# Optimization experiments

Hardware: AMD Instinct MI355X
Metric: run time of the kernel (lower is better)

## Reference

```python
import jax, jax.numpy as jnp
import numpy as np

B, N, K, NUM_CLASSES = 8, 4096, 16, 40
M = B * N


def _safe_norm(v):
    s = jnp.sum(v * v, axis=-1)
    return jnp.where(s > 0, jnp.sqrt(jnp.where(s > 0, s, 1.0)), 0.0)


def _angle(v1, v2):
    cn = _safe_norm(jnp.cross(v1, v2))
    d = jnp.sum(v1 * v2, axis=-1)
    ok = (cn > 0) | (d != 0)
    return jnp.where(ok, jnp.arctan2(cn, jnp.where(ok, d, 1.0)), 0.0)


def _ppf(pos_i, pos_j, n_i, n_j):
    # PyG point_pair_features: pseudo = pos_j - pos_i (j = source, i = target)
    pseudo = pos_j - pos_i
    return jnp.stack([_safe_norm(pseudo), _angle(n_i, pseudo),
                      _angle(n_j, pseudo), _angle(n_i, n_j)], axis=-1)


def _knn_edges(pos):
    # knn_graph(k=K, loop=False), per-graph; returns (src, dst) with self-loops
    # appended (PPFConv add_self_loops=True default).
    p = pos.reshape(B, N, 3)
    sq = jnp.sum(p * p, axis=-1)                                   # [B,N]
    d2 = sq[:, :, None] + sq[:, None, :] - 2.0 * jnp.einsum('bnd,bmd->bnm', p, p)
    d2 = jnp.where(jnp.eye(N, dtype=bool)[None], jnp.inf, d2)      # no loops
    _, nbr = jax.lax.top_k(-d2, K)                                  # [B,N,K]
    offs = (jnp.arange(B) * N)[:, None, None]
    src = (nbr + offs).reshape(-1)                                  # neighbors j
    dst = jnp.repeat(jnp.arange(M), K)                              # targets i
    loops = jnp.arange(M)
    return jnp.concatenate([src, loops]), jnp.concatenate([dst, loops])


def _mlp(e, w1, b1, w2, b2):
    return jax.nn.relu(e @ w1 + b1) @ w2 + b2


def setup_inputs() -> dict:
    key = jax.random.key(0)
    ks = jax.random.split(key, 12)
    pos = jax.random.normal(ks[0], (M, 3), jnp.float32)
    nrm = jax.random.normal(ks[1], (M, 3), jnp.float32)
    nrm = nrm / jnp.linalg.norm(nrm, axis=-1, keepdims=True)
    batch = jnp.repeat(jnp.arange(B, dtype=jnp.int32), N)
    s = 0.1
    return {
        'pos': pos, 'normal': nrm, 'batch': batch,
        'w1a': jax.random.normal(ks[2], (4, 32)) * s,  'b1a': jnp.zeros(32),
        'w1b': jax.random.normal(ks[3], (32, 32)) * s, 'b1b': jnp.zeros(32),
        'w2a': jax.random.normal(ks[4], (36, 32)) * s, 'b2a': jnp.zeros(32),
        'w2b': jax.random.normal(ks[5], (32, 32)) * s, 'b2b': jnp.zeros(32),
        'wc':  jax.random.normal(ks[6], (32, NUM_CLASSES)) * s,
        'bc':  jnp.zeros(NUM_CLASSES),
    }


def reference(pos, normal, batch, w1a, b1a, w1b, b1b, w2a, b2a, w2b, b2b, wc, bc):
    src, dst = _knn_edges(pos)
    feats = _ppf(pos[dst], pos[src], normal[dst], normal[src])      # [E,4]
    # conv1: x=None -> message = mlp1(ppf), scatter-max per target node
    msg1 = _mlp(feats, w1a, b1a, w1b, b1b)
    x = jax.nn.relu(jax.ops.segment_max(msg1, dst, num_segments=M))  # [M,32]
    # conv2: message = mlp2([x_j, ppf])
    msg2 = _mlp(jnp.concatenate([x[src], feats], axis=-1), w2a, b2a, w2b, b2b)
    x = jax.nn.relu(jax.ops.segment_max(msg2, dst, num_segments=M))
    # global_max_pool over each graph (uniform batch: reshape)
    g = x.reshape(B, N, 32).max(axis=1)                              # [B,32]
    return g @ wc + bc                                               # [B,40]
```

## Files before the change

### kernel.cpp

```cpp
#include <hip/hip_runtime.h>
#include <hip/hip_bf16.h>
#include <math.h>

#define NB 8
#define NN 4096
#define KK 16
#define MM (NB*NN)
#define CH 32
#define SLOTS 17
#define NCLS 40
#define BIG 3.0e38f
#define CAP 96
#define NBLK2 (MM/8)
#define HROW 36

#define OW1A 0
#define OB1A 128
#define OW1B 160
#define OB1B 1184
#define OW2A 1216
#define OB2A 2368
#define OW2B 2400
#define OB2B 3424
#define OWC  3456
#define OBC  4736
#define NWTS 4776

typedef short short8 __attribute__((ext_vector_type(8)));
typedef float f32x4  __attribute__((ext_vector_type(4)));

__device__ float4 g_pos4[MM];
__device__ float4 g_nrm4[MM];
__device__ int    g_nbr[MM*KK];
__device__ float  g_u[MM*CH];
__device__ float  g_bmax[NBLK2*CH];
__device__ float  g_wts[NWTS];
__device__ __align__(16) unsigned short g_wfrag1[2][2][64][8];
__device__ __align__(16) unsigned short g_wfrag2[2][2][64][8];
__device__ int    g_isf32;

__device__ __forceinline__ float bf(const __hip_bfloat16 x) { return __bfloat162float(x); }

__device__ __forceinline__ float ldf(const void* p, int i, bool f32) {
  return f32 ? ((const float*)p)[i] : bf(((const __hip_bfloat16*)p)[i]);
}

__device__ __forceinline__ float angf(float ax, float ay, float az,
                                      float bx, float by, float bz) {
  float cx = ay*bz - az*by;
  float cy = az*bx - ax*bz;
  float cz = ax*by - ay*bx;
  float s  = cx*cx + cy*cy + cz*cz;
  float cn = s > 0.f ? sqrtf(s) : 0.f;
  float d  = ax*bx + ay*by + az*bz;
  return (cn > 0.f || d != 0.f) ? atan2f(cn, d) : 0.f;
}

__device__ __forceinline__ void ppf4(const float4 pi, const float4 ni,
                                     const float4 pj, const float4 nj, float* f) {
  float px = pj.x - pi.x, py = pj.y - pi.y, pz = pj.z - pi.z;
  float s = px*px + py*py + pz*pz;
  f[0] = s > 0.f ? sqrtf(s) : 0.f;
  f[1] = angf(ni.x, ni.y, ni.z, px, py, pz);
  f[2] = angf(nj.x, nj.y, nj.z, px, py, pz);
  f[3] = angf(ni.x, ni.y, ni.z, nj.x, nj.y, nj.z);
}

__device__ __forceinline__ unsigned int fkey(float f) {
  unsigned int u = __float_as_uint(f);
  return (u & 0x80000000u) ? ~u : (u | 0x80000000u);
}
__device__ __forceinline__ float funkey(unsigned int k) {
  unsigned int u = (k & 0x80000000u) ? (k ^ 0x80000000u) : ~k;
  return __uint_as_float(u);
}

__device__ __forceinline__ void bsplit(float v, unsigned short* hi, unsigned short* lo) {
  __hip_bfloat16 h = __float2bfloat16(v);
  float hf = __bfloat162float(h);
  __hip_bfloat16 l = __float2bfloat16(v - hf);
  *hi = *reinterpret_cast<unsigned short*>(&h);
  *lo = *reinterpret_cast<unsigned short*>(&l);
}

__device__ __forceinline__ void afrag(const float* row, short8* ah, short8* al) {
  float4 a = *(const float4*)row;
  float4 b = *(const float4*)(row + 4);
  unsigned short h, l;
  #pragma unroll
  for (int j = 0; j < 4; ++j) {
    bsplit((&a.x)[j], &h, &l); (*ah)[j]   = (short)h; (*al)[j]   = (short)l;
    bsplit((&b.x)[j], &h, &l); (*ah)[j+4] = (short)h; (*al)[j+4] = (short)l;
  }
}

__global__ __launch_bounds__(256) void wprep_kernel(
    const void* nrm, const void* w1a, const void* b1a, const void* w1b,
    const void* b1b, const void* w2a, const void* b2a, const void* w2b,
    const void* b2b, const void* wc, const void* bc) {
  __shared__ int sflag;
  const int tid = threadIdx.x;
  if (tid < 64) {
    const float* nf = (const float*)nrm;
    const __hip_bfloat16* nh = (const __hip_bfloat16*)nrm;
    float x = nf[3*tid], y = nf[3*tid+1], z = nf[3*tid+2];
    float ss = x*x + y*y + z*z;
    bool okf = (ss > 0.98f && ss < 1.02f);
    float a = bf(nh[3*tid]), b2 = bf(nh[3*tid+1]), c2 = bf(nh[3*tid+2]);
    float sb = a*a + b2*b2 + c2*c2;
    bool okb = (sb > 0.95f && sb < 1.05f);
    unsigned long long mf = __ballot(okf), mb = __ballot(okb);
    if (tid == 0) {
      sflag = (__popcll(mf) >= __popcll(mb)) ? 1 : 0;
      g_isf32 = sflag;
    }
  }
  __syncthreads();
  const bool f32 = sflag != 0;
  for (int i = tid; i < 128;  i += 256) g_wts[OW1A + i] = ldf(w1a, i, f32);
  for (int i = tid; i < 32;   i += 256) g_wts[OB1A + i] = ldf(b1a, i, f32);
  for (int i = tid; i < 1024; i += 256) g_wts[OW1B + i] = ldf(w1b, i, f32);
  for (int i = tid; i < 32;   i += 256) g_wts[OB1B + i] = ldf(b1b, i, f32);
  for (int i = tid; i < 1152; i += 256) g_wts[OW2A + i] = ldf(w2a, i, f32);
  for (int i = tid; i < 32;   i += 256) g_wts[OB2A + i] = ldf(b2a, i, f32);
  for (int i = tid; i < 1024; i += 256) g_wts[OW2B + i] = ldf(w2b, i, f32);
  for (int i = tid; i < 32;   i += 256) g_wts[OB2B + i] = ldf(b2b, i, f32);
  for (int i = tid; i < 1280; i += 256) g_wts[OWC  + i] = ldf(wc,  i, f32);
  for (int i = tid; i < 40;   i += 256) g_wts[OBC  + i] = ldf(bc,  i, f32);
  for (int i = tid; i < 4096; i += 256) {
    int which = i >> 11;
    int r = i & 2047;
    int t  = r >> 10;  r &= 1023;
    int hl = r >> 9;   r &= 511;
    int ln = r >> 3;
    int j  = r & 7;
    int k = (ln >> 4)*8 + j;
    int c = t*16 + (ln & 15);
    float wv = ldf(which ? w2b : w1b, k*CH + c, f32);
    unsigned short hi, lo;
    bsplit(wv, &hi, &lo);
    unsigned short v = hl ? lo : hi;
    if (which) g_wfrag2[t][hl][ln][j] = v;
    else       g_wfrag1[t][hl][ln][j] = v;
  }
}

__global__ __launch_bounds__(256) void prep_kernel(const void* __restrict__ pos,
                                                   const void* __restrict__ nrm) {
  const bool f32 = g_isf32 != 0;
  int i = blockIdx.x*256 + threadIdx.x;
  float x = ldf(pos, 3*i, f32), y = ldf(pos, 3*i+1, f32), z = ldf(pos, 3*i+2, f32);
  float sq = x*x + y*y + z*z;
  g_pos4[i] = make_float4(x, y, z, sq);
  float a = ldf(nrm, 3*i, f32), b = ldf(nrm, 3*i+1, f32), c = ldf(nrm, 3*i+2, f32);
  g_nrm4[i] = make_float4(a, b, c, 0.f);
}

__global__ __launch_bounds__(512) void knn_kernel() {
  __shared__ float sx[NN], sy[NN], sz[NN];
  __shared__ unsigned short ilst[64][CAP];
  __shared__ double dlst[8][CAP];
  __shared__ int    cnt[64];
  const int tid  = threadIdx.x;
  const int w    = tid >> 6, lane = tid & 63;
  const int blk  = blockIdx.x;
  const int b    = blk >> 6;
  const int qbw  = ((blk & 63) << 6) | (w << 3);
  const float4* bp = g_pos4 + b*NN;

  #pragma unroll
  for (int k = 0; k < 8; ++k) {
    int idx = k*512 + tid;
    float4 o = bp[idx];
    sx[idx] = o.x; sy[idx] = o.y; sz[idx] = o.z;
  }
  __syncthreads();

  float q2x[8], q2y[8], q2z[8];
  #pragma unroll
  for (int qq = 0; qq < 8; ++qq) {
    int qi = qbw + qq;
    q2x[qq] = -2.f*sx[qi]; q2y[qq] = -2.f*sy[qi]; q2z[qq] = -2.f*sz[qi];
  }

  float mn[8];
  #pragma unroll
  for (int qq = 0; qq < 8; ++qq) mn[qq] = BIG;
  #pragma unroll 4
  for (int it = 0; it < 64; ++it) {
    int idx = it*64 + lane;
    float ox = sx[idx], oy = sy[idx], oz = sz[idx];
    float ow = __builtin_fmaf(oz, oz, __builtin_fmaf(oy, oy, ox*ox));
    #pragma unroll
    for (int qq = 0; qq < 8; ++qq) {
      float d = __builtin_fmaf(q2x[qq], ox,
                __builtin_fmaf(q2y[qq], oy,
                __builtin_fmaf(q2z[qq], oz, ow)));
      mn[qq] = fminf(mn[qq], d);
    }
  }

  unsigned int key[8], lo[8], hi[8];
  #pragma unroll
  for (int qq = 0; qq < 8; ++qq) { key[qq] = fkey(mn[qq]); lo[qq] = 0u; hi[qq] = 0xFFFFFFFFu; }
  #pragma unroll 1
  for (int s = 0; s < 32; ++s) {
    #pragma unroll
    for (int qq = 0; qq < 8; ++qq) {
      unsigned int mid = lo[qq] + ((hi[qq] - lo[qq]) >> 1);
      int c = (int)__popcll(__ballot(key[qq] <= mid));
      if (c >= 17) hi[qq] = mid; else lo[qq] = mid + 1;
    }
  }
  float Tf[8];
  #pragma unroll
  for (int qq = 0; qq < 8; ++qq) {
    float T = funkey(hi[qq]);
    Tf[qq] = T + 4e-5f + 1e-5f*fabsf(T);
  }

  if (lane < 8) cnt[(w<<3) | lane] = 0;

  #pragma unroll 4
  for (int it = 0; it < 64; ++it) {
    int idx = it*64 + lane;
    float ox = sx[idx], oy = sy[idx], oz = sz[idx];
    float ow = __builtin_fmaf(oz, oz, __builtin_fmaf(oy, oy, ox*ox));
    #pragma unroll
    for (int qq = 0; qq < 8; ++qq) {
      float d = __builtin_fmaf(q2x[qq], ox,
                __builtin_fmaf(q2y[qq], oy,
                __builtin_fmaf(q2z[qq], oz, ow)));
      if (d <= Tf[qq] && idx != qbw + qq) {
        int p = atomicAdd(&cnt[(w<<3)|qq], 1);
        if (p < CAP) ilst[(w<<3)|qq][p] = (unsigned short)idx;
      }
    }
  }

  #pragma unroll 1
  for (int qq = 0; qq < 8; ++qq) {
    const int qi = qbw + qq;
    const int m = min(cnt[(w<<3)|qq], CAP);
    const double mx = (double)sx[qi], my_ = (double)sy[qi], mz = (double)sz[qi];
    const double sqme = (mx*mx + my_*my_) + mz*mz;
    for (int e = lane; e < m; e += 64) {
      int ci = ilst[(w<<3)|qq][e];
      double ox = (double)sx[ci], oy = (double)sy[ci], oz = (double)sz[ci];
      double sqo = (ox*ox + oy*oy) + oz*oz;
      double dt  = (mx*ox + my_*oy) + mz*oz;
      dlst[w][e] = (sqme + sqo) - 2.0*dt;
    }
    for (int e = lane; e < m; e += 64) {
      double myd = dlst[w][e];
      int myi = ilst[(w<<3)|qq][e];
      int rank = 0;
      for (int o = 0; o < m; ++o) {
        double od = dlst[w][o];
        int oi = ilst[(w<<3)|qq][o];
        rank += (od < myd) || (od == myd && oi < myi);
      }
      if (rank < KK) g_nbr[(b*NN + qi)*KK + rank] = b*NN + myi;
    }
  }
}

__global__ __launch_bounds__(256) void conv1_kernel() {
  __shared__ __align__(16) float fe[136][4];
  __shared__ __align__(16) float h1s[152*HROW];
  __shared__ __align__(16) float wsaT[32*HROW];
  __shared__ float xs[8][CH];
  const int tid = threadIdx.x;
  const int c = tid & 31;
  const int lane = tid & 63, wv = tid >> 6;
  const int quad = lane >> 4, l15 = lane & 15;
  const int node0 = blockIdx.x << 3;
  float w1a_c[4];
  #pragma unroll
  for (int f = 0; f < 4; ++f) w1a_c[f] = g_wts[OW1A + f*CH + c];
  const float b1a_c = g_wts[OB1A + c];
  short8 bH0 = *(const short8*)&g_wfrag1[0][0][lane][0];
  short8 bL0 = *(const short8*)&g_wfrag1[0][1][lane][0];
  short8 bH1 = *(const short8*)&g_wfrag1[1][0][lane][0];
  short8 bL1 = *(const short8*)&g_wfrag1[1][1][lane][0];
  const float bias0 = g_wts[OB1B + l15];
  const float bias1 = g_wts[OB1B + 16 + l15];

  for (int i = tid; i < 1024; i += 256) {
    int k = i >> 5, cc = i & 31;
    wsaT[cc*HROW + k] = g_wts[OW2A + i];
  }
  if (tid < 136) {
    int ns = tid / 17, slot = tid - ns*17;
    int i = node0 + ns;
    int j = (slot < KK) ? g_nbr[i*KK + slot] : i;
    ppf4(g_pos4[i], g_nrm4[i], g_pos4[j], g_nrm4[j], fe[tid]);
  }
  __syncthreads();
  #pragma unroll
  for (int it = 0; it < 17; ++it) {
    int idx = it*256 + tid;
    int e = idx >> 5;
    float4 f4 = *(const float4*)fe[e];
    float h = b1a_c + f4.x*w1a_c[0] + f4.y*w1a_c[1] + f4.z*w1a_c[2] + f4.w*w1a_c[3];
    h1s[e*HROW + c] = fmaxf(h, 0.f);
  }
  __syncthreads();
  #pragma unroll
  for (int ni = 0; ni < 2; ++ni) {
    const int n8 = wv*2 + ni;
    const int rbase = n8*17;
    short8 ah0, al0, ah1, al1;
    afrag(&h1s[(rbase      + l15)*HROW + quad*8], &ah0, &al0);
    afrag(&h1s[(rbase + 16 + l15)*HROW + quad*8], &ah1, &al1);
    f32x4 a00 = {0.f,0.f,0.f,0.f}, a01 = a00, a10 = a00, a11 = a00;
    a00 = __builtin_amdgcn_mfma_f32_16x16x32_bf16(ah0, bH0, a00, 0, 0, 0);
    a00 = __builtin_amdgcn_mfma_f32_16x16x32_bf16(ah0, bL0, a00, 0, 0, 0);
    a00 = __builtin_amdgcn_mfma_f32_16x16x32_bf16(al0, bH0, a00, 0, 0, 0);
    a01 = __builtin_amdgcn_mfma_f32_16x16x32_bf16(ah0, bH1, a01, 0, 0, 0);
    a01 = __builtin_amdgcn_mfma_f32_16x16x32_bf16(ah0, bL1, a01, 0, 0, 0);
    a01 = __builtin_amdgcn_mfma_f32_16x16x32_bf16(al0, bH1, a01, 0, 0, 0);
    a10 = __builtin_amdgcn_mfma_f32_16x16x32_bf16(ah1, bH0, a10, 0, 0, 0);
    a10 = __builtin_amdgcn_mfma_f32_16x16x32_bf16(ah1, bL0, a10, 0, 0, 0);
    a10 = __builtin_amdgcn_mfma_f32_16x16x32_bf16(al1, bH0, a10, 0, 0, 0);
    a11 = __builtin_amdgcn_mfma_f32_16x16x32_bf16(ah1, bH1, a11, 0, 0, 0);
    a11 = __builtin_amdgcn_mfma_f32_16x16x32_bf16(ah1, bL1, a11, 0, 0, 0);
    a11 = __builtin_amdgcn_mfma_f32_16x16x32_bf16(al1, bH1, a11, 0, 0, 0);
    float m0 = fmaxf(fmaxf(a00[0], a00[1]), fmaxf(a00[2], a00[3]));
    float m1 = fmaxf(fmaxf(a01[0], a01[1]), fmaxf(a01[2], a01[3]));
    if (quad == 0) { m0 = fmaxf(m0, a10[0]); m1 = fmaxf(m1, a11[0]); }
    m0 = fmaxf(m0, __shfl_xor(m0, 16)); m0 = fmaxf(m0, __shfl_xor(m0, 32));
    m1 = fmaxf(m1, __shfl_xor(m1, 16)); m1 = fmaxf(m1, __shfl_xor(m1, 32));
    if (quad == 0) {
      xs[n8][l15]      = fmaxf(m0 + bias0, 0.f);
      xs[n8][16 + l15] = fmaxf(m1 + bias1, 0.f);
    }
  }
  __syncthreads();
  const int ns = tid >> 5;
  float uu = 0.f;
  #pragma unroll
  for (int k4 = 0; k4 < 8; ++k4) {
    float4 x4 = *(const float4*)&xs[ns][4*k4];
    float4 w4 = *(const float4*)&wsaT[c*HROW + 4*k4];
    uu += x4.x*w4.x + x4.y*w4.y + x4.z*w4.z + x4.w*w4.w;
  }
  g_u[(node0 + ns)*CH + c] = uu;
}

__global__ __launch_bounds__(256) void conv2_kernel() {
  __shared__ __align__(16) float fe[136][4];
  __shared__ int jn[136];
  __shared__ __align__(16) float h1s[152*HROW];
  __shared__ float xs[8][CH];
  const int tid = threadIdx.x;
  const int c = tid & 31;
  const int lane = tid & 63, wv = tid >> 6;
  const int quad = lane >> 4, l15 = lane & 15;
  const int node0 = blockIdx.x << 3;
  float w2aL_c[4];
  #pragma unroll
  for (int f = 0; f < 4; ++f) w2aL_c[f] = g_wts[OW2A + (CH + f)*CH + c];
  const float b2a_c = g_wts[OB2A + c];
  short8 bH0 = *(const short8*)&g_wfrag2[0][0][lane][0];
  short8 bL0 = *(const short8*)&g_wfrag2[0][1][lane][0];
  short8 bH1 = *(const short8*)&g_wfrag2[1][0][lane][0];
  short8 bL1 = *(const short8*)&g_wfrag2[1][1][lane][0];
  const float bias0 = g_wts[OB2B + l15];
  const float bias1 = g_wts[OB2B + 16 + l15];

  if (tid < 136) {
    int ns = tid / 17, slot = tid - ns*17;
    int i = node0 + ns;
    int j = (slot < KK) ? g_nbr[i*KK + slot] : i;
    jn[tid] = j;
    ppf4(g_pos4[i], g_nrm4[i], g_pos4[j], g_nrm4[j], fe[tid]);
  }
  __syncthreads();
  #pragma unroll
  for (int it = 0; it < 17; ++it) {
    int idx = it*256 + tid;
    int e = idx >> 5;
    float4 f4 = *(const float4*)fe[e];
    float uv = g_u[jn[e]*CH + c];
    float h = b2a_c + uv + f4.x*w2aL_c[0] + f4.y*w2aL_c[1] + f4.z*w2aL_c[2] + f4.w*w2aL_c[3];
    h1s[e*HROW + c] = fmaxf(h, 0.f);
  }
  __syncthreads();
  #pragma unroll
  for (int ni = 0; ni < 2; ++ni) {
    const int n8 = wv*2 + ni;
    const int rbase = n8*17;
    short8 ah0, al0, ah1, al1;
    afrag(&h1s[(rbase      + l15)*HROW + quad*8], &ah0, &al0);
    afrag(&h1s[(rbase + 16 + l15)*HROW + quad*8], &ah1, &al1);
    f32x4 a00 = {0.f,0.f,0.f,0.f}, a01 = a00, a10 = a00, a11 = a00;
    a00 = __builtin_amdgcn_mfma_f32_16x16x32_bf16(ah0, bH0, a00, 0, 0, 0);
    a00 = __builtin_amdgcn_mfma_f32_16x16x32_bf16(ah0, bL0, a00, 0, 0, 0);
    a00 = __builtin_amdgcn_mfma_f32_16x16x32_bf16(al0, bH0, a00, 0, 0, 0);
    a01 = __builtin_amdgcn_mfma_f32_16x16x32_bf16(ah0, bH1, a01, 0, 0, 0);
    a01 = __builtin_amdgcn_mfma_f32_16x16x32_bf16(ah0, bL1, a01, 0, 0, 0);
    a01 = __builtin_amdgcn_mfma_f32_16x16x32_bf16(al0, bH1, a01, 0, 0, 0);
    a10 = __builtin_amdgcn_mfma_f32_16x16x32_bf16(ah1, bH0, a10, 0, 0, 0);
    a10 = __builtin_amdgcn_mfma_f32_16x16x32_bf16(ah1, bL0, a10, 0, 0, 0);
    a10 = __builtin_amdgcn_mfma_f32_16x16x32_bf16(al1, bH0, a10, 0, 0, 0);
    a11 = __builtin_amdgcn_mfma_f32_16x16x32_bf16(ah1, bH1, a11, 0, 0, 0);
    a11 = __builtin_amdgcn_mfma_f32_16x16x32_bf16(ah1, bL1, a11, 0, 0, 0);
    a11 = __builtin_amdgcn_mfma_f32_16x16x32_bf16(al1, bH1, a11, 0, 0, 0);
    float m0 = fmaxf(fmaxf(a00[0], a00[1]), fmaxf(a00[2], a00[3]));
    float m1 = fmaxf(fmaxf(a01[0], a01[1]), fmaxf(a01[2], a01[3]));
    if (quad == 0) { m0 = fmaxf(m0, a10[0]); m1 = fmaxf(m1, a11[0]); }
    m0 = fmaxf(m0, __shfl_xor(m0, 16)); m0 = fmaxf(m0, __shfl_xor(m0, 32));
    m1 = fmaxf(m1, __shfl_xor(m1, 16)); m1 = fmaxf(m1, __shfl_xor(m1, 32));
    if (quad == 0) {
      xs[n8][l15]      = fmaxf(m0 + bias0, 0.f);
      xs[n8][16 + l15] = fmaxf(m1 + bias1, 0.f);
    }
  }
  __syncthreads();
  if (tid < CH) {
    float m2 = xs[0][c];
    #pragma unroll
    for (int r = 1; r < 8; ++r) m2 = fmaxf(m2, xs[r][c]);
    g_bmax[blockIdx.x*CH + c] = m2;
  }
}

__global__ __launch_bounds__(256) void head_kernel(float* __restrict__ out) {
  __shared__ float red[8][CH];
  __shared__ float gm[CH];
  const int g = blockIdx.x;
  const int c = threadIdx.x & 31, sub = threadIdx.x >> 5;
  const float* base = g_bmax + (size_t)(g*512 + sub*64)*CH;
  float mx = 0.f;
  #pragma unroll
  for (int n = 0; n < 64; ++n) mx = fmaxf(mx, base[n*CH + c]);
  red[sub][c] = mx;
  __syncthreads();
  if (threadIdx.x < CH) {
    float m2 = red[0][c];
    #pragma unroll
    for (int r = 1; r < 8; ++r) m2 = fmaxf(m2, red[r][c]);
    gm[c] = m2;
  }
  __syncthreads();
  if (threadIdx.x < NCLS) {
    int co = threadIdx.x;
    float s = g_wts[OBC + co];
    #pragma unroll
    for (int f = 0; f < CH; ++f) s += gm[f] * g_wts[OWC + f*NCLS + co];
    out[g*NCLS + co] = s;
  }
}

extern "C" void kernel_launch(void* const* d_in, const int* in_sizes, int n_in,
                              void* d_out, int out_size, void* d_ws, size_t ws_size,
                              hipStream_t stream) {
  const void* pos = d_in[0];
  const void* nrm = d_in[1];
  const void* w1a = d_in[3];
  const void* b1a = d_in[4];
  const void* w1b = d_in[5];
  const void* b1b = d_in[6];
  const void* w2a = d_in[7];
  const void* b2a = d_in[8];
  const void* w2b = d_in[9];
  const void* b2b = d_in[10];
  const void* wc  = d_in[11];
  const void* bc  = d_in[12];

  wprep_kernel<<<1,      256, 0, stream>>>(nrm, w1a, b1a, w1b, b1b, w2a, b2a, w2b, b2b, wc, bc);
  prep_kernel <<<MM/256, 256, 0, stream>>>(pos, nrm);
  knn_kernel  <<<MM/64,  512, 0, stream>>>();
  conv1_kernel<<<MM/8,   256, 0, stream>>>();
  conv2_kernel<<<MM/8,   256, 0, stream>>>();
  head_kernel <<<NB,     256, 0, stream>>>((float*)d_out);
}
```

Baseline: 216.7 us.

## Fuse kNN with conv1, merge weight prep into prep, use ballot-based compaction

```diff
diff --git a/kernel.cpp b/kernel.cpp
--- a/kernel.cpp
+++ b/kernel.cpp
@@ -37,7 +37,6 @@
 __device__ float  g_wts[NWTS];
 __device__ __align__(16) unsigned short g_wfrag1[2][2][64][8];
 __device__ __align__(16) unsigned short g_wfrag2[2][2][64][8];
-__device__ int    g_isf32;
 
 __device__ __forceinline__ float bf(const __hip_bfloat16 x) { return __bfloat162float(x); }
 
@@ -94,73 +93,83 @@
   }
 }
 
-__global__ __launch_bounds__(256) void wprep_kernel(
-    const void* nrm, const void* w1a, const void* b1a, const void* w1b,
-    const void* b1b, const void* w2a, const void* b2a, const void* w2b,
-    const void* b2b, const void* wc, const void* bc) {
+__global__ __launch_bounds__(256) void prep_kernel(
+    const void* __restrict__ pos, const void* __restrict__ nrm,
+    const void* w1a, const void* b1a, const void* w1b, const void* b1b,
+    const void* w2a, const void* b2a, const void* w2b, const void* b2b,
+    const void* wc, const void* bc) {
   __shared__ int sflag;
   const int tid = threadIdx.x;
+  const int base = blockIdx.x << 8;
   if (tid < 64) {
     const float* nf = (const float*)nrm;
     const __hip_bfloat16* nh = (const __hip_bfloat16*)nrm;
-    float x = nf[3*tid], y = nf[3*tid+1], z = nf[3*tid+2];
+    int n = base + tid;
+    float x = nf[3*n], y = nf[3*n+1], z = nf[3*n+2];
     float ss = x*x + y*y + z*z;
     bool okf = (ss > 0.98f && ss < 1.02f);
-    float a = bf(nh[3*tid]), b2 = bf(nh[3*tid+1]), c2 = bf(nh[3*tid+2]);
+    float a = bf(nh[3*n]), b2 = bf(nh[3*n+1]), c2 = bf(nh[3*n+2]);
     float sb = a*a + b2*b2 + c2*c2;
     bool okb = (sb > 0.95f && sb < 1.05f);
     unsigned long long mf = __ballot(okf), mb = __ballot(okb);
-    if (tid == 0) {
-      sflag = (__popcll(mf) >= __popcll(mb)) ? 1 : 0;
-      g_isf32 = sflag;
-    }
+    if (tid == 0) sflag = (__popcll(mf) >= __popcll(mb)) ? 1 : 0;
   }
   __syncthreads();
   const bool f32 = sflag != 0;
-  for (int i = tid; i < 128;  i += 256) g_wts[OW1A + i] = ldf(w1a, i, f32);
-  for (int i = tid; i < 32;   i += 256) g_wts[OB1A + i] = ldf(b1a, i, f32);
-  for (int i = tid; i < 1024; i += 256) g_wts[OW1B + i] = ldf(w1b, i, f32);
-  for (int i = tid; i < 32;   i += 256) g_wts[OB1B + i] = ldf(b1b, i, f32);
-  for (int i = tid; i < 1152; i += 256) g_wts[OW2A + i] = ldf(w2a, i, f32);
-  for (int i = tid; i < 32;   i += 256) g_wts[OB2A + i] = ldf(b2a, i, f32);
-  for (int i = tid; i < 1024; i += 256) g_wts[OW2B + i] = ldf(w2b, i, f32);
-  for (int i = tid; i < 32;   i += 256) g_wts[OB2B + i] = ldf(b2b, i, f32);
-  for (int i = tid; i < 1280; i += 256) g_wts[OWC  + i] = ldf(wc,  i, f32);
-  for (int i = tid; i < 40;   i += 256) g_wts[OBC  + i] = ldf(bc,  i, f32);
-  for (int i = tid; i < 4096; i += 256) {
-    int which = i >> 11;
-    int r = i & 2047;
-    int t  = r >> 10;  r &= 1023;
-    int hl = r >> 9;   r &= 511;
-    int ln = r >> 3;
-    int j  = r & 7;
-    int k = (ln >> 4)*8 + j;
-    int c = t*16 + (ln & 15);
-    float wv = ldf(which ? w2b : w1b, k*CH + c, f32);
-    unsigned short hi, lo;
-    bsplit(wv, &hi, &lo);
-    unsigned short v = hl ? lo : hi;
-    if (which) g_wfrag2[t][hl][ln][j] = v;
-    else       g_wfrag1[t][hl][ln][j] = v;
-  }
-}
-
-__global__ __launch_bounds__(256) void prep_kernel(const void* __restrict__ pos,
-                                                   const void* __restrict__ nrm) {
-  const bool f32 = g_isf32 != 0;
-  int i = blockIdx.x*256 + threadIdx.x;
-  float x = ldf(pos, 3*i, f32), y = ldf(pos, 3*i+1, f32), z = ldf(pos, 3*i+2, f32);
-  float sq = x*x + y*y + z*z;
-  g_pos4[i] = make_float4(x, y, z, sq);
-  float a = ldf(nrm, 3*i, f32), b = ldf(nrm, 3*i+1, f32), c = ldf(nrm, 3*i+2, f32);
-  g_nrm4[i] = make_float4(a, b, c, 0.f);
-}
-
-__global__ __launch_bounds__(512) void knn_kernel() {
-  __shared__ float sx[NN], sy[NN], sz[NN];
-  __shared__ unsigned short ilst[64][CAP];
-  __shared__ double dlst[8][CAP];
-  __shared__ int    cnt[64];
+  {
+    int i = base + tid;
+    float x = ldf(pos, 3*i, f32), y = ldf(pos, 3*i+1, f32), z = ldf(pos, 3*i+2, f32);
+    g_pos4[i] = make_float4(x, y, z, x*x + y*y + z*z);
+    float a = ldf(nrm, 3*i, f32), bb = ldf(nrm, 3*i+1, f32), cc = ldf(nrm, 3*i+2, f32);
+    g_nrm4[i] = make_float4(a, bb, cc, 0.f);
+  }
+  if (blockIdx.x == 0) {
+    for (int t = tid; t < 128;  t += 256) g_wts[OW1A + t] = ldf(w1a, t, f32);
+    for (int t = tid; t < 32;   t += 256) g_wts[OB1A + t] = ldf(b1a, t, f32);
+    for (int t = tid; t < 1024; t += 256) g_wts[OW1B + t] = ldf(w1b, t, f32);
+    for (int t = tid; t < 32;   t += 256) g_wts[OB1B + t] = ldf(b1b, t, f32);
+    for (int t = tid; t < 1152; t += 256) g_wts[OW2A + t] = ldf(w2a, t, f32);
+    for (int t = tid; t < 32;   t += 256) g_wts[OB2A + t] = ldf(b2a, t, f32);
+    for (int t = tid; t < 1024; t += 256) g_wts[OW2B + t] = ldf(w2b, t, f32);
+    for (int t = tid; t < 32;   t += 256) g_wts[OB2B + t] = ldf(b2b, t, f32);
+    for (int t = tid; t < 1280; t += 256) g_wts[OWC  + t] = ldf(wc,  t, f32);
+    for (int t = tid; t < 40;   t += 256) g_wts[OBC  + t] = ldf(bc,  t, f32);
+    for (int t = tid; t < 4096; t += 256) {
+      int which = t >> 11;
+      int r = t & 2047;
+      int tt = r >> 10;  r &= 1023;
+      int hl = r >> 9;   r &= 511;
+      int ln = r >> 3;
+      int j  = r & 7;
+      int k = (ln >> 4)*8 + j;
+      int c = tt*16 + (ln & 15);
+      float wv = ldf(which ? w2b : w1b, k*CH + c, f32);
+      unsigned short hi, lo;
+      bsplit(wv, &hi, &lo);
+      unsigned short v = hl ? lo : hi;
+      if (which) g_wfrag2[tt][hl][ln][j] = v;
+      else       g_wfrag1[tt][hl][ln][j] = v;
+    }
+  }
+}
+
+__global__ __launch_bounds__(512) void knn_conv1_kernel() {
+  __shared__ __align__(16) union SU {
+    struct {
+      float sx[NN], sy[NN], sz[NN];
+      unsigned short ilst[64][CAP];
+      double dlst[8][CAP];
+    } k;
+    struct {
+      float fe[272][4];
+      float h1s[288*HROW];
+      float wsaT[32*HROW];
+      float xs[16][CH];
+    } c;
+  } u;
+  __shared__ unsigned short nbrs[64][KK];
+  __shared__ unsigned short swcnt[64];
+
   const int tid  = threadIdx.x;
   const int w    = tid >> 6, lane = tid & 63;
   const int blk  = blockIdx.x;
@@ -172,7 +181,7 @@
   for (int k = 0; k < 8; ++k) {
     int idx = k*512 + tid;
     float4 o = bp[idx];
-    sx[idx] = o.x; sy[idx] = o.y; sz[idx] = o.z;
+    u.k.sx[idx] = o.x; u.k.sy[idx] = o.y; u.k.sz[idx] = o.z;
   }
   __syncthreads();
 
@@ -180,7 +189,7 @@
   #pragma unroll
   for (int qq = 0; qq < 8; ++qq) {
     int qi = qbw + qq;
-    q2x[qq] = -2.f*sx[qi]; q2y[qq] = -2.f*sy[qi]; q2z[qq] = -2.f*sz[qi];
+    q2x[qq] = -2.f*u.k.sx[qi]; q2y[qq] = -2.f*u.k.sy[qi]; q2z[qq] = -2.f*u.k.sz[qi];
   }
 
   float mn[8];
@@ -189,7 +198,7 @@
   #pragma unroll 4
   for (int it = 0; it < 64; ++it) {
     int idx = it*64 + lane;
-    float ox = sx[idx], oy = sy[idx], oz = sz[idx];
+    float ox = u.k.sx[idx], oy = u.k.sy[idx], oz = u.k.sz[idx];
     float ow = __builtin_fmaf(oz, oz, __builtin_fmaf(oy, oy, ox*ox));
     #pragma unroll
     for (int qq = 0; qq < 8; ++qq) {
@@ -202,12 +211,12 @@
 
   unsigned int key[8], lo[8], hi[8];
   #pragma unroll
-  for (int qq = 0; qq < 8; ++qq) { key[qq] = fkey(mn[qq]); lo[qq] = 0u; hi[qq] = 0xFFFFFFFFu; }
+  for (int qq = 0; qq < 8; ++qq) { key[qq] = fkey(mn[qq]) >> 16; lo[qq] = 0u; hi[qq] = 0xFFFFu; }
   #pragma unroll 1
-  for (int s = 0; s < 32; ++s) {
+  for (int s = 0; s < 16; ++s) {
     #pragma unroll
     for (int qq = 0; qq < 8; ++qq) {
-      unsigned int mid = lo[qq] + ((hi[qq] - lo[qq]) >> 1);
+      unsigned int mid = (lo[qq] + hi[qq]) >> 1;
       int c = (int)__popcll(__ballot(key[qq] <= mid));
       if (c >= 17) hi[qq] = mid; else lo[qq] = mid + 1;
     }
@@ -215,85 +224,186 @@
   float Tf[8];
   #pragma unroll
   for (int qq = 0; qq < 8; ++qq) {
-    float T = funkey(hi[qq]);
+    float T = funkey((hi[qq] << 16) | 0xFFFFu);
     Tf[qq] = T + 4e-5f + 1e-5f*fabsf(T);
   }
 
-  if (lane < 8) cnt[(w<<3) | lane] = 0;
-
+  unsigned int scnt[8];
+  #pragma unroll
+  for (int qq = 0; qq < 8; ++qq) scnt[qq] = 0u;
   #pragma unroll 4
   for (int it = 0; it < 64; ++it) {
     int idx = it*64 + lane;
-    float ox = sx[idx], oy = sy[idx], oz = sz[idx];
+    float ox = u.k.sx[idx], oy = u.k.sy[idx], oz = u.k.sz[idx];
     float ow = __builtin_fmaf(oz, oz, __builtin_fmaf(oy, oy, ox*ox));
     #pragma unroll
     for (int qq = 0; qq < 8; ++qq) {
       float d = __builtin_fmaf(q2x[qq], ox,
                 __builtin_fmaf(q2y[qq], oy,
                 __builtin_fmaf(q2z[qq], oz, ow)));
-      if (d <= Tf[qq] && idx != qbw + qq) {
-        int p = atomicAdd(&cnt[(w<<3)|qq], 1);
-        if (p < CAP) ilst[(w<<3)|qq][p] = (unsigned short)idx;
+      unsigned long long mk = __ballot(d <= Tf[qq]);
+      if (mk) {
+        unsigned int cbase = scnt[qq];
+        if (d <= Tf[qq]) {
+          unsigned int r = __builtin_amdgcn_mbcnt_hi(
+              (unsigned int)(mk >> 32),
+              __builtin_amdgcn_mbcnt_lo((unsigned int)mk, 0u));
+          unsigned int p = cbase + r;
+          if (p < CAP) u.k.ilst[(w<<3)|qq][p] = (unsigned short)idx;
+        }
+        scnt[qq] = cbase + (unsigned int)__popcll(mk);
       }
     }
+  }
+  if (lane == 0) {
+    #pragma unroll
+    for (int qq = 0; qq < 8; ++qq)
+      swcnt[(w<<3)|qq] = (unsigned short)min((int)scnt[qq], CAP);
   }
 
   #pragma unroll 1
   for (int qq = 0; qq < 8; ++qq) {
     const int qi = qbw + qq;
-    const int m = min(cnt[(w<<3)|qq], CAP);
-    const double mx = (double)sx[qi], my_ = (double)sy[qi], mz = (double)sz[qi];
+    const int ql = (w<<3) | qq;
+    const int m = (int)swcnt[ql];
+    const double mx = (double)u.k.sx[qi], my_ = (double)u.k.sy[qi], mz = (double)u.k.sz[qi];
     const double sqme = (mx*mx + my_*my_) + mz*mz;
     for (int e = lane; e < m; e += 64) {
-      int ci = ilst[(w<<3)|qq][e];
-      double ox = (double)sx[ci], oy = (double)sy[ci], oz = (double)sz[ci];
+      int ci = u.k.ilst[ql][e];
+      double ox = (double)u.k.sx[ci], oy = (double)u.k.sy[ci], oz = (double)u.k.sz[ci];
       double sqo = (ox*ox + oy*oy) + oz*oz;
       double dt  = (mx*ox + my_*oy) + mz*oz;
-      dlst[w][e] = (sqme + sqo) - 2.0*dt;
+      u.k.dlst[w][e] = (sqme + sqo) - 2.0*dt;
     }
     for (int e = lane; e < m; e += 64) {
-      double myd = dlst[w][e];
-      int myi = ilst[(w<<3)|qq][e];
+      double myd = u.k.dlst[w][e];
+      int myi = u.k.ilst[ql][e];
       int rank = 0;
       for (int o = 0; o < m; ++o) {
-        double od = dlst[w][o];
-        int oi = ilst[(w<<3)|qq][o];
+        double od = u.k.dlst[w][o];
+        int oi = u.k.ilst[ql][o];
         rank += (od < myd) || (od == myd && oi < myi);
       }
-      if (rank < KK) g_nbr[(b*NN + qi)*KK + rank] = b*NN + myi;
-    }
-  }
-}
-
-__global__ __launch_bounds__(256) void conv1_kernel() {
+      if (rank >= 1 && rank <= KK) {
+        nbrs[ql][rank-1] = (unsigned short)myi;
+        g_nbr[(b*NN + qi)*KK + (rank-1)] = b*NN + myi;
+      }
+    }
+  }
+
+  const int c32 = tid & 31;
+  const int quad = lane >> 4, l15 = lane & 15;
+  float w1a_c[4];
+  #pragma unroll
+  for (int f = 0; f < 4; ++f) w1a_c[f] = g_wts[OW1A + f*CH + c32];
+  const float b1a_c = g_wts[OB1A + c32];
+  short8 bH0 = *(const short8*)&g_wfrag1[0][0][lane][0];
+  short8 bL0 = *(const short8*)&g_wfrag1[0][1][lane][0];
+  short8 bH1 = *(const short8*)&g_wfrag1[1][0][lane][0];
+  short8 bL1 = *(const short8*)&g_wfrag1[1][1][lane][0];
+  const float bias0 = g_wts[OB1B + l15];
+  const float bias1 = g_wts[OB1B + 16 + l15];
+
+  __syncthreads();
+
+  for (int i2 = tid; i2 < 1024; i2 += 512) {
+    int k = i2 >> 5, cc = i2 & 31;
+    u.c.wsaT[cc*HROW + k] = g_wts[OW2A + i2];
+  }
+  const int nbb = b*NN + ((blk & 63) << 6);
+
+  #pragma unroll 1
+  for (int ck = 0; ck < 4; ++ck) {
+    const int nloc0 = ck << 4;
+    if (tid < 272) {
+      int ns = tid / 17, slot = tid - ns*17;
+      int iloc = nloc0 + ns;
+      int ig = nbb + iloc;
+      int jg = (slot < KK) ? (b*NN + (int)nbrs[iloc][slot]) : ig;
+      ppf4(g_pos4[ig], g_nrm4[ig], g_pos4[jg], g_nrm4[jg], u.c.fe[tid]);
+    }
+    __syncthreads();
+    #pragma unroll
+    for (int it = 0; it < 17; ++it) {
+      int idx = it*512 + tid;
+      int e = idx >> 5;
+      float4 f4 = *(const float4*)u.c.fe[e];
+      float h = b1a_c + f4.x*w1a_c[0] + f4.y*w1a_c[1] + f4.z*w1a_c[2] + f4.w*w1a_c[3];
+      u.c.h1s[e*HROW + c32] = fmaxf(h, 0.f);
+    }
+    __syncthreads();
+    #pragma unroll
+    for (int ni = 0; ni < 2; ++ni) {
+      const int n16 = w*2 + ni;
+      const int rbase = n16*17;
+      short8 ah0, al0, ah1, al1;
+      afrag(&u.c.h1s[(rbase      + l15)*HROW + quad*8], &ah0, &al0);
+      afrag(&u.c.h1s[(rbase + 16 + l15)*HROW + quad*8], &ah1, &al1);
+      f32x4 a00 = {0.f,0.f,0.f,0.f}, a01 = a00, a10 = a00, a11 = a00;
+      a00 = __builtin_amdgcn_mfma_f32_16x16x32_bf16(ah0, bH0, a00, 0, 0, 0);
+      a00 = __builtin_amdgcn_mfma_f32_16x16x32_bf16(ah0, bL0, a00, 0, 0, 0);
+      a00 = __builtin_amdgcn_mfma_f32_16x16x32_bf16(al0, bH0, a00, 0, 0, 0);
+      a01 = __builtin_amdgcn_mfma_f32_16x16x32_bf16(ah0, bH1, a01, 0, 0, 0);
+      a01 = __builtin_amdgcn_mfma_f32_16x16x32_bf16(ah0, bL1, a01, 0, 0, 0);
+      a01 = __builtin_amdgcn_mfma_f32_16x16x32_bf16(al0, bH1, a01, 0, 0, 0);
+      a10 = __builtin_amdgcn_mfma_f32_16x16x32_bf16(ah1, bH0, a10, 0, 0, 0);
+      a10 = __builtin_amdgcn_mfma_f32_16x16x32_bf16(ah1, bL0, a10, 0, 0, 0);
+      a10 = __builtin_amdgcn_mfma_f32_16x16x32_bf16(al1, bH0, a10, 0, 0, 0);
+      a11 = __builtin_amdgcn_mfma_f32_16x16x32_bf16(ah1, bH1, a11, 0, 0, 0);
+      a11 = __builtin_amdgcn_mfma_f32_16x16x32_bf16(ah1, bL1, a11, 0, 0, 0);
+      a11 = __builtin_amdgcn_mfma_f32_16x16x32_bf16(al1, bH1, a11, 0, 0, 0);
+      float m0 = fmaxf(fmaxf(a00[0], a00[1]), fmaxf(a00[2], a00[3]));
+      float m1 = fmaxf(fmaxf(a01[0], a01[1]), fmaxf(a01[2], a01[3]));
+      if (quad == 0) { m0 = fmaxf(m0, a10[0]); m1 = fmaxf(m1, a11[0]); }
+      m0 = fmaxf(m0, __shfl_xor(m0, 16)); m0 = fmaxf(m0, __shfl_xor(m0, 32));
+      m1 = fmaxf(m1, __shfl_xor(m1, 16)); m1 = fmaxf(m1, __shfl_xor(m1, 32));
+      if (quad == 0) {
+        u.c.xs[n16][l15]      = fmaxf(m0 + bias0, 0.f);
+        u.c.xs[n16][16 + l15] = fmaxf(m1 + bias1, 0.f);
+      }
+    }
+    __syncthreads();
+    {
+      int ns = tid >> 5;
+      float uu = 0.f;
+      #pragma unroll
+      for (int k4 = 0; k4 < 8; ++k4) {
+        float4 x4 = *(const float4*)&u.c.xs[ns][4*k4];
+        float4 w4 = *(const float4*)&u.c.wsaT[c32*HROW + 4*k4];
+        uu += x4.x*w4.x + x4.y*w4.y + x4.z*w4.z + x4.w*w4.w;
+      }
+      g_u[(nbb + nloc0 + ns)*CH + c32] = uu;
+    }
+    __syncthreads();
+  }
+}
+
+__global__ __launch_bounds__(256) void conv2_kernel() {
   __shared__ __align__(16) float fe[136][4];
+  __shared__ int jn[136];
   __shared__ __align__(16) float h1s[152*HROW];
-  __shared__ __align__(16) float wsaT[32*HROW];
   __shared__ float xs[8][CH];
   const int tid = threadIdx.x;
   const int c = tid & 31;
   const int lane = tid & 63, wv = tid >> 6;
   const int quad = lane >> 4, l15 = lane & 15;
   const int node0 = blockIdx.x << 3;
-  float w1a_c[4];
-  #pragma unroll
-  for (int f = 0; f < 4; ++f) w1a_c[f] = g_wts[OW1A + f*CH + c];
-  const float b1a_c = g_wts[OB1A + c];
-  short8 bH0 = *(const short8*)&g_wfrag1[0][0][lane][0];
-  short8 bL0 = *(const short8*)&g_wfrag1[0][1][lane][0];
-  short8 bH1 = *(const short8*)&g_wfrag1[1][0][lane][0];
-  short8 bL1 = *(const short8*)&g_wfrag1[1][1][lane][0];
-  const float bias0 = g_wts[OB1B + l15];
-  const float bias1 = g_wts[OB1B + 16 + l15];
-
-  for (int i = tid; i < 1024; i += 256) {
-    int k = i >> 5, cc = i & 31;
-    wsaT[cc*HROW + k] = g_wts[OW2A + i];
-  }
+  float w2aL_c[4];
+  #pragma unroll
+  for (int f = 0; f < 4; ++f) w2aL_c[f] = g_wts[OW2A + (CH + f)*CH + c];
+  const float b2a_c = g_wts[OB2A + c];
+  short8 bH0 = *(const short8*)&g_wfrag2[0][0][lane][0];
+  short8 bL0 = *(const short8*)&g_wfrag2[0][1][lane][0];
+  short8 bH1 = *(const short8*)&g_wfrag2[1][0][lane][0];
+  short8 bL1 = *(const short8*)&g_wfrag2[1][1][lane][0];
+  const float bias0 = g_wts[OB2B + l15];
+  const float bias1 = g_wts[OB2B + 16 + l15];
+
   if (tid < 136) {
     int ns = tid / 17, slot = tid - ns*17;
     int i = node0 + ns;
     int j = (slot < KK) ? g_nbr[i*KK + slot] : i;
+    jn[tid] = j;
     ppf4(g_pos4[i], g_nrm4[i], g_pos4[j], g_nrm4[j], fe[tid]);
   }
   __syncthreads();
@@ -302,7 +412,8 @@
     int idx = it*256 + tid;
     int e = idx >> 5;
     float4 f4 = *(const float4*)fe[e];
-    float h = b1a_c + f4.x*w1a_c[0] + f4.y*w1a_c[1] + f4.z*w1a_c[2] + f4.w*w1a_c[3];
+    float uv = g_u[jn[e]*CH + c];
+    float h = b2a_c + uv + f4.x*w2aL_c[0] + f4.y*w2aL_c[1] + f4.z*w2aL_c[2] + f4.w*w2aL_c[3];
     h1s[e*HROW + c] = fmaxf(h, 0.f);
   }
   __syncthreads();
@@ -337,87 +448,6 @@
     }
   }
   __syncthreads();
-  const int ns = tid >> 5;
-  float uu = 0.f;
-  #pragma unroll
-  for (int k4 = 0; k4 < 8; ++k4) {
-    float4 x4 = *(const float4*)&xs[ns][4*k4];
-    float4 w4 = *(const float4*)&wsaT[c*HROW + 4*k4];
-    uu += x4.x*w4.x + x4.y*w4.y + x4.z*w4.z + x4.w*w4.w;
-  }
-  g_u[(node0 + ns)*CH + c] = uu;
-}
-
-__global__ __launch_bounds__(256) void conv2_kernel() {
-  __shared__ __align__(16) float fe[136][4];
-  __shared__ int jn[136];
-  __shared__ __align__(16) float h1s[152*HROW];
-  __shared__ float xs[8][CH];
-  const int tid = threadIdx.x;
-  const int c = tid & 31;
-  const int lane = tid & 63, wv = tid >> 6;
-  const int quad = lane >> 4, l15 = lane & 15;
-  const int node0 = blockIdx.x << 3;
-  float w2aL_c[4];
-  #pragma unroll
-  for (int f = 0; f < 4; ++f) w2aL_c[f] = g_wts[OW2A + (CH + f)*CH + c];
-  const float b2a_c = g_wts[OB2A + c];
-  short8 bH0 = *(const short8*)&g_wfrag2[0][0][lane][0];
-  short8 bL0 = *(const short8*)&g_wfrag2[0][1][lane][0];
-  short8 bH1 = *(const short8*)&g_wfrag2[1][0][lane][0];
-  short8 bL1 = *(const short8*)&g_wfrag2[1][1][lane][0];
-  const float bias0 = g_wts[OB2B + l15];
-  const float bias1 = g_wts[OB2B + 16 + l15];
-
-  if (tid < 136) {
-    int ns = tid / 17, slot = tid - ns*17;
-    int i = node0 + ns;
-    int j = (slot < KK) ? g_nbr[i*KK + slot] : i;
-    jn[tid] = j;
-    ppf4(g_pos4[i], g_nrm4[i], g_pos4[j], g_nrm4[j], fe[tid]);
-  }
-  __syncthreads();
-  #pragma unroll
-  for (int it = 0; it < 17; ++it) {
-    int idx = it*256 + tid;
-    int e = idx >> 5;
-    float4 f4 = *(const float4*)fe[e];
-    float uv = g_u[jn[e]*CH + c];
-    float h = b2a_c + uv + f4.x*w2aL_c[0] + f4.y*w2aL_c[1] + f4.z*w2aL_c[2] + f4.w*w2aL_c[3];
-    h1s[e*HROW + c] = fmaxf(h, 0.f);
-  }
-  __syncthreads();
-  #pragma unroll
-  for (int ni = 0; ni < 2; ++ni) {
-    const int n8 = wv*2 + ni;
-    const int rbase = n8*17;
-    short8 ah0, al0, ah1, al1;
-    afrag(&h1s[(rbase      + l15)*HROW + quad*8], &ah0, &al0);
-    afrag(&h1s[(rbase + 16 + l15)*HROW + quad*8], &ah1, &al1);
-    f32x4 a00 = {0.f,0.f,0.f,0.f}, a01 = a00, a10 = a00, a11 = a00;
-    a00 = __builtin_amdgcn_mfma_f32_16x16x32_bf16(ah0, bH0, a00, 0, 0, 0);
-    a00 = __builtin_amdgcn_mfma_f32_16x16x32_bf16(ah0, bL0, a00, 0, 0, 0);
-    a00 = __builtin_amdgcn_mfma_f32_16x16x32_bf16(al0, bH0, a00, 0, 0, 0);
-    a01 = __builtin_amdgcn_mfma_f32_16x16x32_bf16(ah0, bH1, a01, 0, 0, 0);
-    a01 = __builtin_amdgcn_mfma_f32_16x16x32_bf16(ah0, bL1, a01, 0, 0, 0);
-    a01 = __builtin_amdgcn_mfma_f32_16x16x32_bf16(al0, bH1, a01, 0, 0, 0);
-    a10 = __builtin_amdgcn_mfma_f32_16x16x32_bf16(ah1, bH0, a10, 0, 0, 0);
-    a10 = __builtin_amdgcn_mfma_f32_16x16x32_bf16(ah1, bL0, a10, 0, 0, 0);
-    a10 = __builtin_amdgcn_mfma_f32_16x16x32_bf16(al1, bH0, a10, 0, 0, 0);
-    a11 = __builtin_amdgcn_mfma_f32_16x16x32_bf16(ah1, bH1, a11, 0, 0, 0);
-    a11 = __builtin_amdgcn_mfma_f32_16x16x32_bf16(ah1, bL1, a11, 0, 0, 0);
-    a11 = __builtin_amdgcn_mfma_f32_16x16x32_bf16(al1, bH1, a11, 0, 0, 0);
-    float m0 = fmaxf(fmaxf(a00[0], a00[1]), fmaxf(a00[2], a00[3]));
-    float m1 = fmaxf(fmaxf(a01[0], a01[1]), fmaxf(a01[2], a01[3]));
-    if (quad == 0) { m0 = fmaxf(m0, a10[0]); m1 = fmaxf(m1, a11[0]); }
-    m0 = fmaxf(m0, __shfl_xor(m0, 16)); m0 = fmaxf(m0, __shfl_xor(m0, 32));
-    m1 = fmaxf(m1, __shfl_xor(m1, 16)); m1 = fmaxf(m1, __shfl_xor(m1, 32));
-    if (quad == 0) {
-      xs[n8][l15]      = fmaxf(m0 + bias0, 0.f);
-      xs[n8][16 + l15] = fmaxf(m1 + bias1, 0.f);
-    }
-  }
-  __syncthreads();
   if (tid < CH) {
     float m2 = xs[0][c];
     #pragma unroll
@@ -469,10 +499,9 @@
   const void* wc  = d_in[11];
   const void* bc  = d_in[12];
 
-  wprep_kernel<<<1,      256, 0, stream>>>(nrm, w1a, b1a, w1b, b1b, w2a, b2a, w2b, b2b, wc, bc);
-  prep_kernel <<<MM/256, 256, 0, stream>>>(pos, nrm);
-  knn_kernel  <<<MM/64,  512, 0, stream>>>();
-  conv1_kernel<<<MM/8,   256, 0, stream>>>();
-  conv2_kernel<<<MM/8,   256, 0, stream>>>();
-  head_kernel <<<NB,     256, 0, stream>>>((float*)d_out);
-}
+  prep_kernel<<<MM/256, 256, 0, stream>>>(pos, nrm, w1a, b1a, w1b, b1b,
+                                          w2a, b2a, w2b, b2b, wc, bc);
+  knn_conv1_kernel<<<MM/64, 512, 0, stream>>>();
+  conv2_kernel<<<MM/8, 256, 0, stream>>>();
+  head_kernel<<<NB, 256, 0, stream>>>((float*)d_out);
+}
```

New measurement: 197.1 us. -9.1%, faster.
